# Performance work log

Hardware: AMD Instinct MI355X
Metric: run time of the kernel (lower is better)

## Reference

```python
import jax, jax.numpy as jnp
import numpy as np

NUM_HEADS = 12
AGENT_NUM = 49


def _adaptive_pool_matrix(L, out):
    # Replicates torch AdaptiveAvgPool1d: segment i averages indices
    # [floor(i*L/out), ceil((i+1)*L/out)). Fixed small loop over `out`.
    P = np.zeros((out, L), dtype=np.float32)
    for i in range(out):
        s = (i * L) // out
        e = -((-(i + 1) * L) // out)  # ceil((i+1)*L/out)
        P[i, s:e] = 1.0 / (e - s)
    return jnp.asarray(P)


def setup_inputs() -> dict:
    b, n, c = 8, 4097, 768
    key = jax.random.key(0)
    ks = jax.random.split(key, 6)
    x = jax.random.normal(ks[0], (b, n, c), dtype=jnp.float32)
    Wqkv = jax.random.normal(ks[1], (c, 3 * c), dtype=jnp.float32) * 0.02
    Wproj = jax.random.normal(ks[2], (c, c), dtype=jnp.float32) * 0.02
    bproj = jax.random.normal(ks[3], (c,), dtype=jnp.float32) * 0.02
    dwc_w = jax.random.normal(ks[4], (c, 1, 3), dtype=jnp.float32) * 0.02  # depthwise conv1d, groups=c
    dwc_b = jax.random.normal(ks[5], (c,), dtype=jnp.float32) * 0.02
    return {"x": x, "Wqkv": Wqkv, "Wproj": Wproj, "bproj": bproj, "dwc_w": dwc_w, "dwc_b": dwc_b}


def reference(x, Wqkv, Wproj, bproj, dwc_w, dwc_b):
    b, n, c = x.shape
    h, a = NUM_HEADS, AGENT_NUM
    hd = c // h
    scale = hd ** -0.5

    qkv = x @ Wqkv  # [b, n, 3c]
    q, k, v = qkv[..., :c], qkv[..., c:2 * c], qkv[..., 2 * c:]

    # Adaptive avg pool over the first n-1 tokens of q -> agent tokens [b, a, c]
    P = _adaptive_pool_matrix(n - 1, a)  # [a, n-1]
    agent_tokens = jnp.einsum('al,blc->bac', P, q[:, :-1, :])

    # split heads -> [b, h, n, hd] / [b, h, a, hd]
    qh = q.reshape(b, n, h, hd).transpose(0, 2, 1, 3)
    kh = k.reshape(b, n, h, hd).transpose(0, 2, 1, 3)
    vh = v.reshape(b, n, h, hd).transpose(0, 2, 1, 3)
    ah = agent_tokens.reshape(b, a, h, hd).transpose(0, 2, 1, 3)

    # stage 1: agent tokens attend over keys (biases in source are dead code)
    agent_attn = jax.nn.softmax((ah * scale) @ kh.transpose(0, 1, 3, 2), axis=-1)  # [b,h,a,n]
    agent_v = agent_attn @ vh  # [b, h, a, hd]

    # stage 2: queries attend over agent tokens
    q_attn = jax.nn.softmax((qh * scale) @ ah.transpose(0, 1, 3, 2), axis=-1)  # [b,h,n,a]
    out = (q_attn @ agent_v).transpose(0, 2, 1, 3).reshape(b, n, c)  # [b, n, c]

    # depthwise conv1d over v of first n-1 tokens, added back
    v_ = v[:, :-1, :].transpose(0, 2, 1)  # [b, c, n-1]
    dwc = jax.lax.conv_general_dilated(
        v_, dwc_w, window_strides=(1,), padding=((1, 1),),
        feature_group_count=c, dimension_numbers=('NCH', 'OIH', 'NCH'))
    dwc = dwc + dwc_b[None, :, None]
    out = out.at[:, :-1, :].add(dwc.transpose(0, 2, 1))

    # fusion_encoder branch skipped (counter=0 != sorted(first_half)[0]=1)
    return out @ Wproj + bproj
```

## Files before the change

### kernel.cpp

```cpp
#include <hip/hip_runtime.h>

namespace {

constexpr int Bb = 8;
constexpr int Nn = 4097;
constexpr int Cc = 768;
constexpr int Hh = 12;
constexpr int HD = 64;
constexpr int Aa = 49;
constexpr int LDQ = 3 * Cc;
constexpr int NCH = 16;
constexpr int CHUNK = 256;
constexpr float SCALE = 0.125f;
constexpr int KP = 1536;
constexpr int KA = 768;

typedef short s16x8 __attribute__((ext_vector_type(8)));
typedef float f32x4 __attribute__((ext_vector_type(4)));

struct HL { short h, l; };

__device__ inline HL splitbf(float v) {
  unsigned u = __float_as_uint(v);
  HL r;
  r.h = (short)(u >> 16);
  float hf = __uint_as_float(u & 0xffff0000u);
  float lf = v - hf;
  unsigned ul = __float_as_uint(lf);
  r.l = (short)((ul + 0x7fffu + ((ul >> 16) & 1u)) >> 16);
  return r;
}

__device__ inline short bf16rne(float v) {
  unsigned u = __float_as_uint(v);
  return (short)((u + 0x7fffu + ((u >> 16) & 1u)) >> 16);
}
__device__ inline float bf2f(unsigned short s) {
  return __uint_as_float((unsigned)s << 16);
}

__device__ inline void gload16(const short* g, void* l) {
  __builtin_amdgcn_global_load_lds(
      (const __attribute__((address_space(1))) void*)g,
      (__attribute__((address_space(3))) void*)l, 16, 0, 0);
}


__global__ __launch_bounds__(256) void pack_act(
    const float* __restrict__ src, short* __restrict__ dst, int M) {
  int idx = blockIdx.x * 256 + threadIdx.x;
  if (idx >= M * 96) return;
  int m = idx / 96, kc = idx - m * 96;
  const float* s = src + (size_t)m * 768 + kc * 8;
  float4 v0 = *(const float4*)s;
  float4 v1 = *(const float4*)(s + 4);
  s16x8 hv;
  hv[0] = bf16rne(v0.x); hv[1] = bf16rne(v0.y);
  hv[2] = bf16rne(v0.z); hv[3] = bf16rne(v0.w);
  hv[4] = bf16rne(v1.x); hv[5] = bf16rne(v1.y);
  hv[6] = bf16rne(v1.z); hv[7] = bf16rne(v1.w);
  int win = (kc >> 3) * 64;
  int jj = ((kc & 7) ^ (m & 7)) * 8;
  *(s16x8*)&dst[(size_t)m * KA + win + jj] = hv;
}

__global__ __launch_bounds__(256) void pack_w(
    const float* __restrict__ W, short* __restrict__ Wpk, int N) {
  int idx = blockIdx.x * 256 + threadIdx.x;
  if (idx >= 96 * N) return;
  int kc = idx / N, n = idx - kc * N;
  s16x8 hv, lv;
#pragma unroll
  for (int i = 0; i < 8; ++i) {
    HL r = splitbf(W[(size_t)(kc * 8 + i) * N + n]);
    hv[i] = r.h; lv[i] = r.l;
  }
  int win = (kc >> 3) * 64;
  int jj = ((kc & 7) ^ (n & 7)) * 8;
  short* d = Wpk + (size_t)n * KP;
  *(s16x8*)&d[win + jj] = hv;
  *(s16x8*)&d[768 + win + jj] = lv;
}

__global__ __launch_bounds__(256) void gemm_pk2(
    const short* __restrict__ Apk, const short* __restrict__ Bpk,
    float* __restrict__ Cm, const float* __restrict__ bias,
    int Mr, int ldc, int nch, int nwg) {
  __shared__ __align__(16) short AsH[128 * 64];
  __shared__ __align__(16) short BsH[128 * 64], BsL[128 * 64];
  const int t = threadIdx.x;
  const int lane = t & 63;
  const int w = t >> 6;
  const int wr = w >> 1, wc = w & 1;
  const int l15 = lane & 15, l4 = lane >> 4;

  const int j = blockIdx.x;
  const int q = nwg >> 3, r = nwg & 7;
  const int xcd = j & 7, pos = j >> 3;
  const int logical =
      (xcd < r ? xcd * (q + 1) : r * (q + 1) + (xcd - r) * q) + pos;
  const int mt = logical / nch, nc = logical - mt * nch;
  const int m0 = mt * 128, n0 = nc * 128;

  f32x4 acc[4][4];
#pragma unroll
  for (int mi = 0; mi < 4; ++mi)
#pragma unroll
    for (int ni = 0; ni < 4; ++ni) acc[mi][ni] = (f32x4){0.f, 0.f, 0.f, 0.f};

  for (int kt = 0; kt < 12; ++kt) {
    const short* Ab = Apk + (size_t)m0 * KA + kt * 64;
    const short* Bt = Bpk + (size_t)n0 * KP + kt * 64;
    __syncthreads();
#pragma unroll
    for (int i = 0; i < 4; ++i) {
      const int o = (i * 256 + t) * 16;
      const int row = o >> 7;
      const int ce = (o & 127) >> 1;
      gload16(Ab + (size_t)row * KA + ce, (char*)AsH + o);
      gload16(Bt + (size_t)row * KP + ce, (char*)BsH + o);
      gload16(Bt + (size_t)row * KP + 768 + ce, (char*)BsL + o);
    }
    __syncthreads();
#pragma unroll
    for (int ks = 0; ks < 2; ++ks) {
      s16x8 ah[4], bh[4], bl[4];
#pragma unroll
      for (int mi = 0; mi < 4; ++mi) {
        int rr = wr * 64 + mi * 16 + l15;
        ah[mi] = *(const s16x8*)&AsH[rr * 64 + ((((ks << 2) + l4) ^ (l15 & 7)) << 3)];
      }
#pragma unroll
      for (int ni = 0; ni < 4; ++ni) {
        int rr = wc * 64 + ni * 16 + l15;
        int off = rr * 64 + ((((ks << 2) + l4) ^ (l15 & 7)) << 3);
        bh[ni] = *(const s16x8*)&BsH[off];
        bl[ni] = *(const s16x8*)&BsL[off];
      }
#pragma unroll
      for (int mi = 0; mi < 4; ++mi)
#pragma unroll
        for (int ni = 0; ni < 4; ++ni) {
          acc[mi][ni] = __builtin_amdgcn_mfma_f32_16x16x32_bf16(
              ah[mi], bh[ni], acc[mi][ni], 0, 0, 0);
          acc[mi][ni] = __builtin_amdgcn_mfma_f32_16x16x32_bf16(
              ah[mi], bl[ni], acc[mi][ni], 0, 0, 0);
        }
    }
  }

#pragma unroll
  for (int mi = 0; mi < 4; ++mi) {
#pragma unroll
    for (int jr = 0; jr < 4; ++jr) {
      int gr = m0 + wr * 64 + mi * 16 + l4 * 4 + jr;
      if (gr < Mr) {
#pragma unroll
        for (int ni = 0; ni < 4; ++ni) {
          int gc = n0 + wc * 64 + ni * 16 + l15;
          float v = acc[mi][ni][jr];
          if (bias) v += bias[gc];
          Cm[(size_t)gr * ldc + gc] = v;
        }
      }
    }
  }
}

__global__ __launch_bounds__(192) void pool_agents(
    const float* __restrict__ qkv, float* __restrict__ at) {
  const int ba = blockIdx.x;
  const int bg = ba / Aa, a = ba % Aa;
  const int s = (a * 4096) / 49;
  const int e = ((a + 1) * 4096 + 48) / 49;
  const float w = 1.0f / (float)(e - s);
  const int c4 = threadIdx.x * 4;
  f32x4 sum = (f32x4){0.f, 0.f, 0.f, 0.f};
#pragma unroll 4
  for (int l = s; l < e; ++l) {
    const float4 v = *(const float4*)&qkv[(size_t)(bg * Nn + l) * LDQ + c4];
    sum[0] += v.x; sum[1] += v.y; sum[2] += v.z; sum[3] += v.w;
  }
  float4 o;
  o.x = sum[0] * w; o.y = sum[1] * w; o.z = sum[2] * w; o.w = sum[3] * w;
  *(float4*)&at[(size_t)(bg * Aa + a) * Cc + c4] = o;
}

__global__ __launch_bounds__(256) void agent_attn_mfma(
    const float* __restrict__ qkv, const float* __restrict__ at,
    float* __restrict__ paccv, float* __restrict__ paccs) {
  const int chunk = blockIdx.x, h = blockIdx.y, bg = blockIdx.z;
  __shared__ __align__(16) short AhH[4096];
  __shared__ __align__(16) short KH[4096];
  __shared__ __align__(16) short VtH[4096];
  const int t = threadIdx.x;
  const int w = t >> 6, lane = t & 63, l15 = lane & 15, l4 = lane >> 4;

  for (int idx = t; idx < 512; idx += 256) {
    int a = idx >> 3, c8 = idx & 7;
    float vals[8];
    if (a < Aa) {
      const float* src = &at[(size_t)(bg * Aa + a) * Cc + h * HD + c8 * 8];
      *(float4*)&vals[0] = *(const float4*)src;
      *(float4*)&vals[4] = *(const float4*)(src + 4);
    } else {
#pragma unroll
      for (int i = 0; i < 8; ++i) vals[i] = 0.f;
    }
    s16x8 hv;
#pragma unroll
    for (int i = 0; i < 8; ++i) hv[i] = bf16rne(vals[i]);
    *(s16x8*)&AhH[a * 64 + ((c8 ^ (a & 7)) << 3)] = hv;
  }

  f32x4 acc[4];
#pragma unroll
  for (int ni = 0; ni < 4; ++ni) acc[ni] = (f32x4){0.f, 0.f, 0.f, 0.f};
  float rs[4] = {0.f, 0.f, 0.f, 0.f};

  const int jstart = chunk * CHUNK;
  const int jend = (chunk == NCH - 1) ? Nn : jstart + CHUNK;
  const int srow = t >> 2, sc0 = (t & 3) * 16;

  for (int j0 = jstart; j0 < jend; j0 += 64) {
    __syncthreads();
    {
      int jg = j0 + srow;
      float kv[16], vv[16];
      if (jg < jend) {
        const float* p = &qkv[(size_t)(bg * Nn + jg) * LDQ + Cc + h * HD + sc0];
#pragma unroll
        for (int r = 0; r < 4; ++r) {
          *(float4*)&kv[r * 4] = *(const float4*)(p + r * 4);
          *(float4*)&vv[r * 4] = *(const float4*)(p + Cc + r * 4);
        }
      } else {
#pragma unroll
        for (int i = 0; i < 16; ++i) { kv[i] = 0.f; vv[i] = 0.f; }
      }
#pragma unroll
      for (int r = 0; r < 2; ++r) {
        s16x8 hv;
#pragma unroll
        for (int i = 0; i < 8; ++i) hv[i] = bf16rne(kv[r * 8 + i]);
        int ch = (sc0 >> 3) + r;
        *(s16x8*)&KH[srow * 64 + ((ch ^ (srow & 7)) << 3)] = hv;
      }
#pragma unroll
      for (int i = 0; i < 16; ++i) {
        int c = sc0 + i;
        VtH[c * 64 + ((((srow >> 3) ^ (c & 7)) << 3)) + (srow & 7)] =
            bf16rne(vv[i]);
      }
    }
    __syncthreads();

    f32x4 s[4];
#pragma unroll
    for (int ni = 0; ni < 4; ++ni) s[ni] = (f32x4){0.f, 0.f, 0.f, 0.f};
#pragma unroll
    for (int ks = 0; ks < 2; ++ks) {
      int sw = (((ks << 2) + l4) ^ (l15 & 7)) << 3;
      s16x8 ahh = *(const s16x8*)&AhH[(w * 16 + l15) * 64 + sw];
#pragma unroll
      for (int ni = 0; ni < 4; ++ni) {
        s16x8 kh = *(const s16x8*)&KH[(ni * 16 + l15) * 64 + sw];
        s[ni] = __builtin_amdgcn_mfma_f32_16x16x32_bf16(ahh, kh, s[ni], 0, 0, 0);
      }
    }
    __syncthreads();

#pragma unroll
    for (int ni = 0; ni < 4; ++ni) {
#pragma unroll
      for (int reg = 0; reg < 4; ++reg) {
        int jj = l15 + 16 * ni;
        float pv = (j0 + jj < jend) ? expf(s[ni][reg] * SCALE) : 0.f;
        rs[reg] += pv;
        int a = w * 16 + l4 * 4 + reg;
        KH[a * 64 + ((((jj >> 3) ^ (a & 7)) << 3)) + (jj & 7)] = bf16rne(pv);
      }
    }

#pragma unroll
    for (int ks = 0; ks < 2; ++ks) {
      int sw = (((ks << 2) + l4) ^ (l15 & 7)) << 3;
      s16x8 ph = *(const s16x8*)&KH[(w * 16 + l15) * 64 + sw];
#pragma unroll
      for (int ni = 0; ni < 4; ++ni) {
        s16x8 vh = *(const s16x8*)&VtH[(ni * 16 + l15) * 64 + sw];
        acc[ni] = __builtin_amdgcn_mfma_f32_16x16x32_bf16(ph, vh, acc[ni], 0, 0, 0);
      }
    }
  }

#pragma unroll
  for (int reg = 0; reg < 4; ++reg) {
    rs[reg] += __shfl_xor(rs[reg], 1);
    rs[reg] += __shfl_xor(rs[reg], 2);
    rs[reg] += __shfl_xor(rs[reg], 4);
    rs[reg] += __shfl_xor(rs[reg], 8);
  }
  const int basev = ((bg * Hh + h) * NCH + chunk) * (Aa * 64);
#pragma unroll
  for (int reg = 0; reg < 4; ++reg) {
    int a = w * 16 + l4 * 4 + reg;
    if (a < Aa) {
#pragma unroll
      for (int ni = 0; ni < 4; ++ni)
        paccv[basev + a * 64 + l15 + 16 * ni] = acc[ni][reg];
      if (l15 == 0)
        paccs[((bg * Hh + h) * NCH + chunk) * Aa + a] = rs[reg];
    }
  }
}

__global__ __launch_bounds__(256) void merge_agent(
    const float* __restrict__ paccv, const float* __restrict__ paccs,
    float* __restrict__ av) {
  const int bh = blockIdx.x;
  const int t = threadIdx.x;
  for (int idx = t; idx < Aa * HD; idx += 256) {
    int a = idx >> 6;
    float vs = 0.f, ss = 0.f;
#pragma unroll
    for (int ch = 0; ch < NCH; ++ch) {
      vs += paccv[(size_t)((bh * NCH + ch)) * (Aa * 64) + idx];
      ss += paccs[(bh * NCH + ch) * Aa + a];
    }
    av[(size_t)bh * (Aa * HD) + idx] = vs / ss;
  }
}

__global__ __launch_bounds__(256) void q_attn_dwc(
    const float* __restrict__ qkv, const float* __restrict__ at,
    const float* __restrict__ av, const float* __restrict__ dwcw,
    const float* __restrict__ dwcb, short* __restrict__ Opk) {
  const int i0 = blockIdx.x * 64, h = blockIdx.y, bg = blockIdx.z;
  __shared__ __align__(16) short SMEM[13568];
  short* AhH = SMEM;
  short* AvH = SMEM + 4096;
  short* QH  = SMEM + 8192;
  const int t = threadIdx.x;
  const int w = t >> 6, lane = t & 63, l15 = lane & 15, l4 = lane >> 4;

  for (int idx = t; idx < 512; idx += 256) {
    int a = idx >> 3, c8 = idx & 7;
    float vah[8], vav[8];
    if (a < Aa) {
      const float* s1 = &at[(size_t)(bg * Aa + a) * Cc + h * HD + c8 * 8];
      const float* s2 = &av[(size_t)(bg * Hh + h) * (Aa * HD) + a * HD + c8 * 8];
      *(float4*)&vah[0] = *(const float4*)s1;
      *(float4*)&vah[4] = *(const float4*)(s1 + 4);
      *(float4*)&vav[0] = *(const float4*)s2;
      *(float4*)&vav[4] = *(const float4*)(s2 + 4);
    } else {
#pragma unroll
      for (int i = 0; i < 8; ++i) { vah[i] = 0.f; vav[i] = 0.f; }
    }
    s16x8 hv;
#pragma unroll
    for (int i = 0; i < 8; ++i) hv[i] = bf16rne(vah[i]);
    *(s16x8*)&AhH[a * 64 + ((c8 ^ (a & 7)) << 3)] = hv;
#pragma unroll
    for (int i = 0; i < 8; ++i) {
      int c = c8 * 8 + i;
      AvH[c * 64 + ((((a >> 3) ^ (c & 7)) << 3)) + (a & 7)] = bf16rne(vav[i]);
    }
  }
  {
    int row = t >> 2, c0 = (t & 3) * 16;
    int ig = i0 + row;
    float qv[16];
    if (ig < Nn) {
      const float* p = &qkv[(size_t)(bg * Nn + ig) * LDQ + h * HD + c0];
#pragma unroll
      for (int r = 0; r < 4; ++r) *(float4*)&qv[r * 4] = *(const float4*)(p + r * 4);
    } else {
#pragma unroll
      for (int i = 0; i < 16; ++i) qv[i] = 0.f;
    }
#pragma unroll
    for (int r = 0; r < 2; ++r) {
      s16x8 hv;
#pragma unroll
      for (int i = 0; i < 8; ++i) hv[i] = bf16rne(qv[r * 8 + i]);
      int ch = (c0 >> 3) + r;
      *(s16x8*)&QH[row * 64 + ((ch ^ (row & 7)) << 3)] = hv;
    }
  }
  __syncthreads();

  f32x4 s[4];
#pragma unroll
  for (int ni = 0; ni < 4; ++ni) s[ni] = (f32x4){0.f, 0.f, 0.f, 0.f};
#pragma unroll
  for (int ks = 0; ks < 2; ++ks) {
    int sw = (((ks << 2) + l4) ^ (l15 & 7)) << 3;
    s16x8 qh = *(const s16x8*)&QH[(w * 16 + l15) * 64 + sw];
#pragma unroll
    for (int ni = 0; ni < 4; ++ni) {
      s16x8 bh = *(const s16x8*)&AhH[(ni * 16 + l15) * 64 + sw];
      s[ni] = __builtin_amdgcn_mfma_f32_16x16x32_bf16(qh, bh, s[ni], 0, 0, 0);
    }
  }
  __syncthreads();

  float rsum[4] = {0.f, 0.f, 0.f, 0.f};
#pragma unroll
  for (int ni = 0; ni < 4; ++ni) {
#pragma unroll
    for (int reg = 0; reg < 4; ++reg) {
      int a = l15 + 16 * ni;
      float pv = (a < Aa) ? expf(s[ni][reg] * SCALE) : 0.f;
      s[ni][reg] = pv;
      rsum[reg] += pv;
    }
  }
#pragma unroll
  for (int reg = 0; reg < 4; ++reg) {
    rsum[reg] += __shfl_xor(rsum[reg], 1);
    rsum[reg] += __shfl_xor(rsum[reg], 2);
    rsum[reg] += __shfl_xor(rsum[reg], 4);
    rsum[reg] += __shfl_xor(rsum[reg], 8);
    rsum[reg] = 1.0f / rsum[reg];
  }
#pragma unroll
  for (int ni = 0; ni < 4; ++ni) {
#pragma unroll
    for (int reg = 0; reg < 4; ++reg) {
      int row = w * 16 + l4 * 4 + reg;
      int a = l15 + 16 * ni;
      QH[row * 64 + ((((a >> 3) ^ (row & 7)) << 3)) + (a & 7)] =
          bf16rne(s[ni][reg] * rsum[reg]);
    }
  }
  __syncthreads();

  f32x4 o[4];
#pragma unroll
  for (int ni = 0; ni < 4; ++ni) o[ni] = (f32x4){0.f, 0.f, 0.f, 0.f};
#pragma unroll
  for (int ks = 0; ks < 2; ++ks) {
    int sw = (((ks << 2) + l4) ^ (l15 & 7)) << 3;
    s16x8 ph = *(const s16x8*)&QH[(w * 16 + l15) * 64 + sw];
#pragma unroll
    for (int ni = 0; ni < 4; ++ni) {
      s16x8 vh = *(const s16x8*)&AvH[(ni * 16 + l15) * 64 + sw];
      o[ni] = __builtin_amdgcn_mfma_f32_16x16x32_bf16(ph, vh, o[ni], 0, 0, 0);
    }
  }
  __syncthreads();

  float* olds = (float*)SMEM;
  unsigned short* vlds = (unsigned short*)(SMEM + 8704);
#pragma unroll
  for (int reg = 0; reg < 4; ++reg) {
    int row = w * 16 + l4 * 4 + reg;
#pragma unroll
    for (int ni = 0; ni < 4; ++ni)
      olds[row * 68 + l15 + 16 * ni] = o[ni][reg];
  }
  constexpr int VLD = 72;
  for (int idx = t; idx < 66 * 16; idx += 256) {
    int row = idx >> 4, cs = (idx & 15) << 2;
    int gr = i0 - 1 + row;
    float4 v = make_float4(0.f, 0.f, 0.f, 0.f);
    if (gr >= 0 && gr < 4096)
      v = *(const float4*)&qkv[((size_t)bg * Nn + gr) * LDQ + 2 * Cc + h * HD + cs];
    unsigned short* d = &vlds[row * VLD + cs];
    d[0] = (unsigned short)bf16rne(v.x); d[1] = (unsigned short)bf16rne(v.y);
    d[2] = (unsigned short)bf16rne(v.z); d[3] = (unsigned short)bf16rne(v.w);
  }
  __syncthreads();

#pragma unroll
  for (int it = 0; it < 2; ++it) {
    int widx = t + it * 256;
    int ml = widx >> 3, kc = widx & 7;
    int ig = i0 + ml;
    if (ig >= Nn) continue;
    float vals[8];
    *(float4*)&vals[0] = *(const float4*)&olds[ml * 68 + kc * 8];
    *(float4*)&vals[4] = *(const float4*)&olds[ml * 68 + kc * 8 + 4];
    if (ig < Nn - 1) {
      const int rl = ml + 1;
      const unsigned short* vr = &vlds[rl * VLD + kc * 8];
#pragma unroll
      for (int cI = 0; cI < 8; ++cI) {
        int cg = h * HD + kc * 8 + cI;
        float vm = bf2f(vr[cI - VLD]);
        float v0 = bf2f(vr[cI]);
        float vp = bf2f(vr[cI + VLD]);
        vals[cI] += dwcw[cg * 3] * vm + dwcw[cg * 3 + 1] * v0 +
                    dwcw[cg * 3 + 2] * vp + dwcb[cg];
      }
    }
    s16x8 hv;
#pragma unroll
    for (int cI = 0; cI < 8; ++cI) hv[cI] = bf16rne(vals[cI]);
    const int mrow = bg * Nn + ig;
    const int win = h * 64;
    const int jj = (kc ^ (mrow & 7)) * 8;
    *(s16x8*)&Opk[(size_t)mrow * KA + win + jj] = hv;
  }
}

}

extern "C" void kernel_launch(void* const* d_in, const int* in_sizes, int n_in,
                              void* d_out, int out_size, void* d_ws,
                              size_t ws_size, hipStream_t stream) {
  const float* x = (const float*)d_in[0];
  const float* Wqkv = (const float*)d_in[1];
  const float* Wproj = (const float*)d_in[2];
  const float* bproj = (const float*)d_in[3];
  const float* dwcw = (const float*)d_in[4];
  const float* dwcb = (const float*)d_in[5];
  float* out = (float*)d_out;

  char* p = (char*)d_ws;
  short* WQpk = (short*)p; p += (size_t)LDQ * KP * 2;
  short* WPpk = (short*)p; p += (size_t)Cc * KP * 2;
  const size_t fixedBytes = (size_t)p - (size_t)d_ws;

  auto bytesFor = [&](int G) -> size_t {
    size_t Mg = (size_t)G * Nn;
    size_t Mpad = ((Mg + 127) / 128) * 128;
    size_t fl = Mg * LDQ +
                (size_t)G * (Aa * Cc + Hh * NCH * Aa * 64 + Hh * NCH * Aa +
                             Hh * Aa * HD);
    return fixedBytes + fl * 4 + Mpad * KA * 2;
  };
  int G = 1;
  for (int g = Bb; g >= 1; --g) {
    if (bytesFor(g) <= ws_size) { G = g; break; }
  }

  const size_t MgMax = (size_t)G * Nn;
  float* qkv = (float*)p;
  float* at = qkv + MgMax * LDQ;
  float* paccv = at + (size_t)G * Aa * Cc;
  float* paccs = paccv + (size_t)G * Hh * NCH * Aa * 64;
  float* av = paccs + (size_t)G * Hh * NCH * Aa;
  short* Apk = (short*)(av + (size_t)G * Hh * Aa * HD);

  dim3 blk(256);
  pack_w<<<dim3((96 * LDQ + 255) / 256), blk, 0, stream>>>(Wqkv, WQpk, LDQ);
  pack_w<<<dim3((96 * Cc + 255) / 256), blk, 0, stream>>>(Wproj, WPpk, Cc);

  for (int b0 = 0; b0 < Bb; b0 += G) {
    const int Gi = (b0 + G <= Bb) ? G : (Bb - b0);
    const int Mg = Gi * Nn;
    const int Mtiles = (Mg + 127) / 128;
    const float* xg = x + (size_t)b0 * Nn * Cc;
    float* outg = out + (size_t)b0 * Nn * Cc;

    pack_act<<<dim3((Mg * 96 + 255) / 256), blk, 0, stream>>>(xg, Apk, Mg);
    {
      const int nch = LDQ / 128;
      const int nwg = Mtiles * nch;
      gemm_pk2<<<dim3(nwg), blk, 0, stream>>>(Apk, WQpk, qkv, nullptr, Mg,
                                              LDQ, nch, nwg);
    }
    pool_agents<<<dim3(Gi * Aa), dim3(192), 0, stream>>>(qkv, at);
    agent_attn_mfma<<<dim3(NCH, Hh, Gi), blk, 0, stream>>>(qkv, at, paccv,
                                                           paccs);
    merge_agent<<<dim3(Gi * Hh), blk, 0, stream>>>(paccv, paccs, av);
    q_attn_dwc<<<dim3((Nn + 63) / 64, Hh, Gi), blk, 0, stream>>>(
        qkv, at, av, dwcw, dwcb, Apk);
    {
      const int nch = Cc / 128;
      const int nwg = Mtiles * nch;
      gemm_pk2<<<dim3(nwg), blk, 0, stream>>>(Apk, WPpk, outg, bproj, Mg,
                                              Cc, nch, nwg);
    }
  }
}
```

Measured before the change: 589.2 us.

## Store QKV intermediate in bf16 instead of fp32 across attention kernels

```diff
diff --git a/kernel.cpp b/kernel.cpp
--- a/kernel.cpp
+++ b/kernel.cpp
@@ -16,6 +16,7 @@
 constexpr int KA = 768;
 
 typedef short s16x8 __attribute__((ext_vector_type(8)));
+typedef short s16x4 __attribute__((ext_vector_type(4)));
 typedef float f32x4 __attribute__((ext_vector_type(4)));
 
 struct HL { short h, l; };
@@ -35,8 +36,8 @@
   unsigned u = __float_as_uint(v);
   return (short)((u + 0x7fffu + ((u >> 16) & 1u)) >> 16);
 }
-__device__ inline float bf2f(unsigned short s) {
-  return __uint_as_float((unsigned)s << 16);
+__device__ inline float bf2f(short s) {
+  return __uint_as_float((unsigned)(unsigned short)s << 16);
 }
 
 __device__ inline void gload16(const short* g, void* l) {
@@ -82,9 +83,10 @@
   *(s16x8*)&d[768 + win + jj] = lv;
 }
 
+template <bool BF16OUT>
 __global__ __launch_bounds__(256) void gemm_pk2(
     const short* __restrict__ Apk, const short* __restrict__ Bpk,
-    float* __restrict__ Cm, const float* __restrict__ bias,
+    void* __restrict__ Cm, const float* __restrict__ bias,
     int Mr, int ldc, int nch, int nwg) {
   __shared__ __align__(16) short AsH[128 * 64];
   __shared__ __align__(16) short BsH[128 * 64], BsL[128 * 64];
@@ -160,7 +162,11 @@
           int gc = n0 + wc * 64 + ni * 16 + l15;
           float v = acc[mi][ni][jr];
           if (bias) v += bias[gc];
-          Cm[(size_t)gr * ldc + gc] = v;
+          if constexpr (BF16OUT) {
+            ((short*)Cm)[(size_t)gr * ldc + gc] = bf16rne(v);
+          } else {
+            ((float*)Cm)[(size_t)gr * ldc + gc] = v;
+          }
         }
       }
     }
@@ -168,7 +174,7 @@
 }
 
 __global__ __launch_bounds__(192) void pool_agents(
-    const float* __restrict__ qkv, float* __restrict__ at) {
+    const short* __restrict__ qkvb, short* __restrict__ atb) {
   const int ba = blockIdx.x;
   const int bg = ba / Aa, a = ba % Aa;
   const int s = (a * 4096) / 49;
@@ -176,18 +182,19 @@
   const float w = 1.0f / (float)(e - s);
   const int c4 = threadIdx.x * 4;
   f32x4 sum = (f32x4){0.f, 0.f, 0.f, 0.f};
-#pragma unroll 4
   for (int l = s; l < e; ++l) {
-    const float4 v = *(const float4*)&qkv[(size_t)(bg * Nn + l) * LDQ + c4];
-    sum[0] += v.x; sum[1] += v.y; sum[2] += v.z; sum[3] += v.w;
-  }
-  float4 o;
-  o.x = sum[0] * w; o.y = sum[1] * w; o.z = sum[2] * w; o.w = sum[3] * w;
-  *(float4*)&at[(size_t)(bg * Aa + a) * Cc + c4] = o;
+    const s16x4 v = *(const s16x4*)&qkvb[(size_t)(bg * Nn + l) * LDQ + c4];
+    sum[0] += bf2f(v[0]); sum[1] += bf2f(v[1]);
+    sum[2] += bf2f(v[2]); sum[3] += bf2f(v[3]);
+  }
+  s16x4 o;
+  o[0] = bf16rne(sum[0] * w); o[1] = bf16rne(sum[1] * w);
+  o[2] = bf16rne(sum[2] * w); o[3] = bf16rne(sum[3] * w);
+  *(s16x4*)&atb[(size_t)(bg * Aa + a) * Cc + c4] = o;
 }
 
 __global__ __launch_bounds__(256) void agent_attn_mfma(
-    const float* __restrict__ qkv, const float* __restrict__ at,
+    const short* __restrict__ qkvb, const short* __restrict__ atb,
     float* __restrict__ paccv, float* __restrict__ paccs) {
   const int chunk = blockIdx.x, h = blockIdx.y, bg = blockIdx.z;
   __shared__ __align__(16) short AhH[4096];
@@ -198,18 +205,9 @@
 
   for (int idx = t; idx < 512; idx += 256) {
     int a = idx >> 3, c8 = idx & 7;
-    float vals[8];
-    if (a < Aa) {
-      const float* src = &at[(size_t)(bg * Aa + a) * Cc + h * HD + c8 * 8];
-      *(float4*)&vals[0] = *(const float4*)src;
-      *(float4*)&vals[4] = *(const float4*)(src + 4);
-    } else {
-#pragma unroll
-      for (int i = 0; i < 8; ++i) vals[i] = 0.f;
-    }
-    s16x8 hv;
-#pragma unroll
-    for (int i = 0; i < 8; ++i) hv[i] = bf16rne(vals[i]);
+    s16x8 hv = (s16x8)(short)0;
+    if (a < Aa)
+      hv = *(const s16x8*)&atb[(size_t)(bg * Aa + a) * Cc + h * HD + c8 * 8];
     *(s16x8*)&AhH[a * 64 + ((c8 ^ (a & 7)) << 3)] = hv;
   }
 
@@ -226,31 +224,26 @@
     __syncthreads();
     {
       int jg = j0 + srow;
-      float kv[16], vv[16];
+      s16x8 k0 = (s16x8)(short)0, k1 = k0, v0 = k0, v1 = k0;
       if (jg < jend) {
-        const float* p = &qkv[(size_t)(bg * Nn + jg) * LDQ + Cc + h * HD + sc0];
-#pragma unroll
-        for (int r = 0; r < 4; ++r) {
-          *(float4*)&kv[r * 4] = *(const float4*)(p + r * 4);
-          *(float4*)&vv[r * 4] = *(const float4*)(p + Cc + r * 4);
-        }
-      } else {
-#pragma unroll
-        for (int i = 0; i < 16; ++i) { kv[i] = 0.f; vv[i] = 0.f; }
-      }
-#pragma unroll
-      for (int r = 0; r < 2; ++r) {
-        s16x8 hv;
-#pragma unroll
-        for (int i = 0; i < 8; ++i) hv[i] = bf16rne(kv[r * 8 + i]);
-        int ch = (sc0 >> 3) + r;
-        *(s16x8*)&KH[srow * 64 + ((ch ^ (srow & 7)) << 3)] = hv;
-      }
-#pragma unroll
-      for (int i = 0; i < 16; ++i) {
+        const short* p = &qkvb[(size_t)(bg * Nn + jg) * LDQ + Cc + h * HD + sc0];
+        k0 = *(const s16x8*)p;
+        k1 = *(const s16x8*)(p + 8);
+        v0 = *(const s16x8*)(p + Cc);
+        v1 = *(const s16x8*)(p + Cc + 8);
+      }
+      int ch = sc0 >> 3;
+      *(s16x8*)&KH[srow * 64 + (((ch + 0) ^ (srow & 7)) << 3)] = k0;
+      *(s16x8*)&KH[srow * 64 + (((ch + 1) ^ (srow & 7)) << 3)] = k1;
+#pragma unroll
+      for (int i = 0; i < 8; ++i) {
         int c = sc0 + i;
-        VtH[c * 64 + ((((srow >> 3) ^ (c & 7)) << 3)) + (srow & 7)] =
-            bf16rne(vv[i]);
+        VtH[c * 64 + ((((srow >> 3) ^ (c & 7)) << 3)) + (srow & 7)] = v0[i];
+      }
+#pragma unroll
+      for (int i = 0; i < 8; ++i) {
+        int c = sc0 + 8 + i;
+        VtH[c * 64 + ((((srow >> 3) ^ (c & 7)) << 3)) + (srow & 7)] = v1[i];
       }
     }
     __syncthreads();
@@ -317,7 +310,7 @@
 
 __global__ __launch_bounds__(256) void merge_agent(
     const float* __restrict__ paccv, const float* __restrict__ paccs,
-    float* __restrict__ av) {
+    short* __restrict__ avb) {
   const int bh = blockIdx.x;
   const int t = threadIdx.x;
   for (int idx = t; idx < Aa * HD; idx += 256) {
@@ -328,13 +321,13 @@
       vs += paccv[(size_t)((bh * NCH + ch)) * (Aa * 64) + idx];
       ss += paccs[(bh * NCH + ch) * Aa + a];
     }
-    av[(size_t)bh * (Aa * HD) + idx] = vs / ss;
+    avb[(size_t)bh * (Aa * HD) + idx] = bf16rne(vs / ss);
   }
 }
 
 __global__ __launch_bounds__(256) void q_attn_dwc(
-    const float* __restrict__ qkv, const float* __restrict__ at,
-    const float* __restrict__ av, const float* __restrict__ dwcw,
+    const short* __restrict__ qkvb, const short* __restrict__ atb,
+    const short* __restrict__ avb, const float* __restrict__ dwcw,
     const float* __restrict__ dwcb, short* __restrict__ Opk) {
   const int i0 = blockIdx.x * 64, h = blockIdx.y, bg = blockIdx.z;
   __shared__ __align__(16) short SMEM[13568];
@@ -346,48 +339,30 @@
 
   for (int idx = t; idx < 512; idx += 256) {
     int a = idx >> 3, c8 = idx & 7;
-    float vah[8], vav[8];
+    s16x8 hv = (s16x8)(short)0, av8 = hv;
     if (a < Aa) {
-      const float* s1 = &at[(size_t)(bg * Aa + a) * Cc + h * HD + c8 * 8];
-      const float* s2 = &av[(size_t)(bg * Hh + h) * (Aa * HD) + a * HD + c8 * 8];
-      *(float4*)&vah[0] = *(const float4*)s1;
-      *(float4*)&vah[4] = *(const float4*)(s1 + 4);
-      *(float4*)&vav[0] = *(const float4*)s2;
-      *(float4*)&vav[4] = *(const float4*)(s2 + 4);
-    } else {
-#pragma unroll
-      for (int i = 0; i < 8; ++i) { vah[i] = 0.f; vav[i] = 0.f; }
-    }
-    s16x8 hv;
-#pragma unroll
-    for (int i = 0; i < 8; ++i) hv[i] = bf16rne(vah[i]);
+      hv = *(const s16x8*)&atb[(size_t)(bg * Aa + a) * Cc + h * HD + c8 * 8];
+      av8 = *(const s16x8*)&avb[(size_t)(bg * Hh + h) * (Aa * HD) + a * HD + c8 * 8];
+    }
     *(s16x8*)&AhH[a * 64 + ((c8 ^ (a & 7)) << 3)] = hv;
 #pragma unroll
     for (int i = 0; i < 8; ++i) {
       int c = c8 * 8 + i;
-      AvH[c * 64 + ((((a >> 3) ^ (c & 7)) << 3)) + (a & 7)] = bf16rne(vav[i]);
+      AvH[c * 64 + ((((a >> 3) ^ (c & 7)) << 3)) + (a & 7)] = av8[i];
     }
   }
   {
     int row = t >> 2, c0 = (t & 3) * 16;
     int ig = i0 + row;
-    float qv[16];
+    s16x8 q0 = (s16x8)(short)0, q1 = q0;
     if (ig < Nn) {
-      const float* p = &qkv[(size_t)(bg * Nn + ig) * LDQ + h * HD + c0];
-#pragma unroll
-      for (int r = 0; r < 4; ++r) *(float4*)&qv[r * 4] = *(const float4*)(p + r * 4);
-    } else {
-#pragma unroll
-      for (int i = 0; i < 16; ++i) qv[i] = 0.f;
-    }
-#pragma unroll
-    for (int r = 0; r < 2; ++r) {
-      s16x8 hv;
-#pragma unroll
-      for (int i = 0; i < 8; ++i) hv[i] = bf16rne(qv[r * 8 + i]);
-      int ch = (c0 >> 3) + r;
-      *(s16x8*)&QH[row * 64 + ((ch ^ (row & 7)) << 3)] = hv;
-    }
+      const short* p = &qkvb[(size_t)(bg * Nn + ig) * LDQ + h * HD + c0];
+      q0 = *(const s16x8*)p;
+      q1 = *(const s16x8*)(p + 8);
+    }
+    int ch = c0 >> 3;
+    *(s16x8*)&QH[row * 64 + (((ch + 0) ^ (row & 7)) << 3)] = q0;
+    *(s16x8*)&QH[row * 64 + (((ch + 1) ^ (row & 7)) << 3)] = q1;
   }
   __syncthreads();
 
@@ -453,7 +428,7 @@
   __syncthreads();
 
   float* olds = (float*)SMEM;
-  unsigned short* vlds = (unsigned short*)(SMEM + 8704);
+  short* vlds = SMEM + 8704;
 #pragma unroll
   for (int reg = 0; reg < 4; ++reg) {
     int row = w * 16 + l4 * 4 + reg;
@@ -465,12 +440,10 @@
   for (int idx = t; idx < 66 * 16; idx += 256) {
     int row = idx >> 4, cs = (idx & 15) << 2;
     int gr = i0 - 1 + row;
-    float4 v = make_float4(0.f, 0.f, 0.f, 0.f);
+    s16x4 v = (s16x4)(short)0;
     if (gr >= 0 && gr < 4096)
-      v = *(const float4*)&qkv[((size_t)bg * Nn + gr) * LDQ + 2 * Cc + h * HD + cs];
-    unsigned short* d = &vlds[row * VLD + cs];
-    d[0] = (unsigned short)bf16rne(v.x); d[1] = (unsigned short)bf16rne(v.y);
-    d[2] = (unsigned short)bf16rne(v.z); d[3] = (unsigned short)bf16rne(v.w);
+      v = *(const s16x4*)&qkvb[((size_t)bg * Nn + gr) * LDQ + 2 * Cc + h * HD + cs];
+    *(s16x4*)&vlds[row * VLD + cs] = v;
   }
   __syncthreads();
 
@@ -485,7 +458,7 @@
     *(float4*)&vals[4] = *(const float4*)&olds[ml * 68 + kc * 8 + 4];
     if (ig < Nn - 1) {
       const int rl = ml + 1;
-      const unsigned short* vr = &vlds[rl * VLD + kc * 8];
+      const short* vr = &vlds[rl * VLD + kc * 8];
 #pragma unroll
       for (int cI = 0; cI < 8; ++cI) {
         int cg = h * HD + kc * 8 + cI;
@@ -527,10 +500,9 @@
   auto bytesFor = [&](int G) -> size_t {
     size_t Mg = (size_t)G * Nn;
     size_t Mpad = ((Mg + 127) / 128) * 128;
-    size_t fl = Mg * LDQ +
-                (size_t)G * (Aa * Cc + Hh * NCH * Aa * 64 + Hh * NCH * Aa +
-                             Hh * Aa * HD);
-    return fixedBytes + fl * 4 + Mpad * KA * 2;
+    size_t fl = (size_t)G * (Hh * NCH * Aa * 64 + Hh * NCH * Aa);
+    size_t sh = Mg * LDQ + (size_t)G * (Aa * Cc + Hh * Aa * HD) + Mpad * KA;
+    return fixedBytes + fl * 4 + sh * 2;
   };
   int G = 1;
   for (int g = Bb; g >= 1; --g) {
@@ -538,12 +510,12 @@
   }
 
   const size_t MgMax = (size_t)G * Nn;
-  float* qkv = (float*)p;
-  float* at = qkv + MgMax * LDQ;
-  float* paccv = at + (size_t)G * Aa * Cc;
+  float* paccv = (float*)p;
   float* paccs = paccv + (size_t)G * Hh * NCH * Aa * 64;
-  float* av = paccs + (size_t)G * Hh * NCH * Aa;
-  short* Apk = (short*)(av + (size_t)G * Hh * Aa * HD);
+  short* qkvb = (short*)(paccs + (size_t)G * Hh * NCH * Aa);
+  short* atb = qkvb + MgMax * LDQ;
+  short* avb = atb + (size_t)G * Aa * Cc;
+  short* Apk = avb + (size_t)G * Hh * Aa * HD;
 
   dim3 blk(256);
   pack_w<<<dim3((96 * LDQ + 255) / 256), blk, 0, stream>>>(Wqkv, WQpk, LDQ);
@@ -560,20 +532,20 @@
     {
       const int nch = LDQ / 128;
       const int nwg = Mtiles * nch;
-      gemm_pk2<<<dim3(nwg), blk, 0, stream>>>(Apk, WQpk, qkv, nullptr, Mg,
-                                              LDQ, nch, nwg);
-    }
-    pool_agents<<<dim3(Gi * Aa), dim3(192), 0, stream>>>(qkv, at);
-    agent_attn_mfma<<<dim3(NCH, Hh, Gi), blk, 0, stream>>>(qkv, at, paccv,
+      gemm_pk2<true><<<dim3(nwg), blk, 0, stream>>>(Apk, WQpk, qkvb, nullptr,
+                                                    Mg, LDQ, nch, nwg);
+    }
+    pool_agents<<<dim3(Gi * Aa), dim3(192), 0, stream>>>(qkvb, atb);
+    agent_attn_mfma<<<dim3(NCH, Hh, Gi), blk, 0, stream>>>(qkvb, atb, paccv,
                                                            paccs);
-    merge_agent<<<dim3(Gi * Hh), blk, 0, stream>>>(paccv, paccs, av);
+    merge_agent<<<dim3(Gi * Hh), blk, 0, stream>>>(paccv, paccs, avb);
     q_attn_dwc<<<dim3((Nn + 63) / 64, Hh, Gi), blk, 0, stream>>>(
-        qkv, at, av, dwcw, dwcb, Apk);
+        qkvb, atb, avb, dwcw, dwcb, Apk);
     {
       const int nch = Cc / 128;
       const int nwg = Mtiles * nch;
-      gemm_pk2<<<dim3(nwg), blk, 0, stream>>>(Apk, WPpk, outg, bproj, Mg,
-                                              Cc, nch, nwg);
-    }
-  }
-}
+      gemm_pk2<false><<<dim3(nwg), blk, 0, stream>>>(Apk, WPpk, outg, bproj,
+                                                     Mg, Cc, nch, nwg);
+    }
+  }
+}
```

After: 524.7 us, median of 2. 10.9% less time.
